# Optimization experiments

Measured on AMD Instinct MI355X. Metric: run time of the kernel, lower is better.

Reference implementation:

```python
import jax, jax.numpy as jnp
import numpy as np

D = 1024
H = 16
DH = D // H  # 64
EPS_LN = 1e-5
CONF_MIN = 1e-6


def sparsemax(z):
    """Sparsemax along the last axis (Martins & Astudillo 2016)."""
    K = z.shape[-1]
    z_sorted = jnp.flip(jnp.sort(z, axis=-1), axis=-1)          # descending
    cssv = jnp.cumsum(z_sorted, axis=-1)                        # cumulative sums
    r = jnp.arange(1, K + 1, dtype=z.dtype)                     # 1..K
    support = (1.0 + r * z_sorted) > cssv                       # bool mask
    k = jnp.sum(support, axis=-1, keepdims=True)                # support size
    tau = (jnp.take_along_axis(cssv, k.astype(jnp.int32) - 1, axis=-1) - 1.0) / k.astype(z.dtype)
    return jnp.maximum(z - tau, 0.0)


def setup_inputs() -> dict:
    key = jax.random.key(0)
    ks = jax.random.split(key, 16)
    B, P, K = 8, 512, 16
    s = 0.02
    return {
        "cell_query": jax.random.normal(ks[0], (B, D), jnp.float32),
        "gene_facets": jax.random.normal(ks[1], (B, P, K, D), jnp.float32),
        "confidence": jax.random.uniform(ks[2], (B, P, K), jnp.float32),
        "wq": jax.random.normal(ks[3], (D, D), jnp.float32) * s,
        "bq": jnp.zeros((D,), jnp.float32),
        "wk": jax.random.normal(ks[4], (D, D), jnp.float32) * s,
        "bk": jnp.zeros((D,), jnp.float32),
        "wv": jax.random.normal(ks[5], (D, D), jnp.float32) * s,
        "bv": jnp.zeros((D,), jnp.float32),
        "wo": jax.random.normal(ks[6], (D, D), jnp.float32) * s,
        "bo": jnp.zeros((D,), jnp.float32),
        "gamma": jnp.ones((D,), jnp.float32),
        "beta": jnp.zeros((D,), jnp.float32),
    }


def reference(cell_query, gene_facets, confidence,
              wq, bq, wk, bk, wv, bv, wo, bo, gamma, beta):
    B = gene_facets.shape[0]
    P = gene_facets.shape[1]
    Kf = gene_facets.shape[2]

    # Projections (torch Linear: x @ W^T + b; here weights stored already transposed as (D,D))
    Q = (cell_query @ wq + bq).reshape(B, H, DH)                       # (B,H,d)
    Kp = (gene_facets @ wk + bk).reshape(B, P, Kf, H, DH)              # (B,P,K,H,d)
    Vp = (gene_facets @ wv + bv).reshape(B, P, Kf, H, DH)              # (B,P,K,H,d)

    # scores: (B,P,H,K)
    scores = jnp.einsum('bhd,bpkhd->bphk', Q, Kp) / jnp.sqrt(jnp.asarray(DH, Q.dtype))
    conf_bias = jnp.log(jnp.clip(confidence, CONF_MIN))                # (B,P,K)
    scores = scores + conf_bias[:, :, None, :]

    alpha = sparsemax(scores)                                          # (B,P,H,K), dropout_p=0 -> identity

    out = jnp.einsum('bphk,bpkhd->bphd', alpha, Vp).reshape(B, P, D)
    out = out @ wo + bo

    # LayerNorm over last dim
    mu = jnp.mean(out, axis=-1, keepdims=True)
    var = jnp.mean((out - mu) ** 2, axis=-1, keepdims=True)
    out = (out - mu) * jax.lax.rsqrt(var + EPS_LN) * gamma + beta
    return out, alpha
```

## Files before the change

kernel.cpp:

```cpp
#include <hip/hip_runtime.h>


typedef float f32x4 __attribute__((ext_vector_type(4)));
typedef short s16x4 __attribute__((ext_vector_type(4)));
typedef short s16x8 __attribute__((ext_vector_type(8)));

__device__ __forceinline__ unsigned short f2bf(float f) {
  unsigned u = __builtin_bit_cast(unsigned, f);
  u = (u + 0x7FFFu + ((u >> 16) & 1u)) >> 16;
  return (unsigned short)u;
}

__device__ __forceinline__ s16x8 pack8(s16x4 lo, s16x4 hi) {
  s16x8 r;
  r[0] = lo[0]; r[1] = lo[1]; r[2] = lo[2]; r[3] = lo[3];
  r[4] = hi[0]; r[5] = hi[1]; r[6] = hi[2]; r[7] = hi[3];
  return r;
}

__global__ __launch_bounds__(256) void k_trans(
    const float* __restrict__ wv, const float* __restrict__ wo,
    unsigned short* __restrict__ wvt, unsigned short* __restrict__ wot) {
  __shared__ float ts[64][65];
  int bid = blockIdx.x;
  const float* src = (bid < 256) ? wv : wo;
  unsigned short* dst = (bid < 256) ? wvt : wot;
  int tile = bid & 255;
  int er = (tile >> 4) << 6;
  int cb = (tile & 15) << 6;
  int t = threadIdx.x;
  int r = t >> 2, c0 = (t & 3) << 4;
#pragma unroll
  for (int j = 0; j < 16; j += 4) {
    f32x4 v = *(const f32x4*)&src[(long)(er + r) * 1024 + cb + c0 + j];
    ts[r][c0 + j + 0] = v[0];
    ts[r][c0 + j + 1] = v[1];
    ts[r][c0 + j + 2] = v[2];
    ts[r][c0 + j + 3] = v[3];
  }
  __syncthreads();
  s16x8 o0, o1;
#pragma unroll
  for (int j = 0; j < 8; ++j) o0[j] = (short)f2bf(ts[c0 + j][r]);
#pragma unroll
  for (int j = 0; j < 8; ++j) o1[j] = (short)f2bf(ts[c0 + 8 + j][r]);
  long ob = (long)(cb + r) * 1024 + er + c0;
  *(s16x8*)&dst[ob] = o0;
  *(s16x8*)&dst[ob + 8] = o1;
}

__global__ __launch_bounds__(256) void k_qpart(
    const float* __restrict__ cq, const float* __restrict__ wq,
    float* __restrict__ qpart) {
  int eq = blockIdx.x, t = threadIdx.x;
  int d0 = t << 2;
  f32x4 acc[8] = {};
  for (int i = 0; i < 64; ++i) {
    int e = (eq << 6) + i;
    f32x4 w = *(const f32x4*)&wq[(long)e * 1024 + d0];
#pragma unroll
    for (int b = 0; b < 8; ++b) acc[b] += w * cq[(b << 10) + e];
  }
#pragma unroll
  for (int b = 0; b < 8; ++b)
    *(f32x4*)&qpart[(long)((b << 4) + eq) * 1024 + d0] = acc[b];
}

__global__ __launch_bounds__(256) void k_wtilde(
    const float* __restrict__ wk, const float* __restrict__ bk,
    const float* __restrict__ bq, const float* __restrict__ qpart,
    unsigned short* __restrict__ wt, float* __restrict__ cvec) {
  __shared__ float Qs[16][68];
  int et = blockIdx.x, b = blockIdx.y, t = threadIdx.x;
#pragma unroll
  for (int j = 0; j < 4; ++j) {
    int d = t + (j << 8);
    float s = bq[d];
    for (int q = 0; q < 16; ++q) s += qpart[(long)((b << 4) + q) * 1024 + d];
    Qs[d >> 6][d & 63] = s;
  }
  __syncthreads();
  int h = t & 15, el = t >> 4;
#pragma unroll
  for (int ii = 0; ii < 8; ++ii) {
    int e = (et << 7) + (ii << 4) + el;
    const float* wr = &wk[(long)e * 1024 + (h << 6)];
    float s = 0.f;
#pragma unroll
    for (int d = 0; d < 64; d += 4) {
      f32x4 w = *(const f32x4*)&wr[d];
      s += w[0] * Qs[h][d] + w[1] * Qs[h][d + 1] + w[2] * Qs[h][d + 2] + w[3] * Qs[h][d + 3];
    }
    wt[(long)((b << 4) + h) * 1024 + e] = f2bf(s);
  }
  if (et == 0 && t < 16) {
    float s = 0.f;
    for (int d = 0; d < 64; ++d) s += bk[(t << 6) + d] * Qs[t][d];
    cvec[(b << 4) + t] = s;
  }
}

#define GSTR 1028
#define TSTR 20
__global__ __launch_bounds__(256, 2) void k_scores(
    const float* __restrict__ G, const float* __restrict__ conf,
    const unsigned short* __restrict__ wt, const float* __restrict__ cvec,
    float* __restrict__ alpha_out, unsigned short* __restrict__ gbar,
    int b0, int hstride) {
  __shared__ short Gs[16 * GSTR];
  __shared__ short Gt[1024 * TSTR];
  __shared__ short As[16 * 32];
  __shared__ float ps[1024];
  __shared__ float lc[16];

  int t = threadIdx.x;
  int lane = t & 63, w = t >> 6;
  int l15 = lane & 15, g4 = lane >> 4;
  int bp = blockIdx.x;
  long gbp = (long)b0 * 512 + bp;
  int b = (int)(gbp >> 9);
  const float* Grow = G + gbp * 16384;
  const unsigned short* wtb = wt + (long)b * 16384;

#pragma unroll
  for (int half = 0; half < 2; ++half) {
    s16x4 col[8];
#pragma unroll
    for (int j = 0; j < 8; ++j) {
      int k = (half << 3) + j;
      f32x4 g = *(const f32x4*)&Grow[(k << 10) + (t << 2)];
      s16x4 h4;
      h4[0] = (short)f2bf(g[0]); h4[1] = (short)f2bf(g[1]);
      h4[2] = (short)f2bf(g[2]); h4[3] = (short)f2bf(g[3]);
      *(s16x4*)&Gs[k * GSTR + (t << 2)] = h4;
      col[j] = h4;
    }
#pragma unroll
    for (int q = 0; q < 4; ++q) {
      int e = (t << 2) + q;
      s16x4 lo, hi;
      lo[0] = col[0][q]; lo[1] = col[1][q]; lo[2] = col[2][q]; lo[3] = col[3][q];
      hi[0] = col[4][q]; hi[1] = col[5][q]; hi[2] = col[6][q]; hi[3] = col[7][q];
      *(s16x4*)&Gt[e * TSTR + (half << 3)] = lo;
      *(s16x4*)&Gt[e * TSTR + (half << 3) + 4] = hi;
    }
  }
  if (t < 16) lc[t] = logf(fmaxf(conf[gbp * 16 + t], 1e-6f));
  __syncthreads();

  f32x4 sc = {0.f, 0.f, 0.f, 0.f};
#pragma unroll
  for (int i = 0; i < 8; ++i) {
    int e0 = (w << 8) + (i << 5) + (g4 << 3);
    s16x8 af = *(const s16x8*)&wtb[l15 * 1024 + e0];
    int off = l15 * GSTR + e0;
    s16x8 bf = pack8(*(const s16x4*)&Gs[off], *(const s16x4*)&Gs[off + 4]);
    sc = __builtin_amdgcn_mfma_f32_16x16x32_bf16(af, bf, sc, 0, 0, 0);
  }
#pragma unroll
  for (int r = 0; r < 4; ++r)
    ps[(w << 8) + ((g4 << 2) + r) * 16 + l15] = sc[r];
  __syncthreads();

  {
    int h = t >> 4, k = t & 15;
    float z = (ps[h * 16 + k] + ps[256 + h * 16 + k] + ps[512 + h * 16 + k] +
               ps[768 + h * 16 + k] + cvec[b * 16 + h]) * 0.125f + lc[k];
    float v = z;
#pragma unroll
    for (int kk = 2; kk <= 16; kk <<= 1) {
#pragma unroll
      for (int j = kk >> 1; j > 0; j >>= 1) {
        float o = __shfl_xor(v, j, 64);
        bool dirDesc = ((l15 & kk) == 0);
        bool takeMax = (((l15 & j) == 0) == dirDesc);
        v = takeMax ? fmaxf(v, o) : fminf(v, o);
      }
    }
    float cs = v;
#pragma unroll
    for (int d = 1; d < 16; d <<= 1) {
      float o = __shfl_up(cs, (unsigned)d, 16);
      if (l15 >= d) cs += o;
    }
    bool sup = (1.0f + (float)(l15 + 1) * v) > cs;
    unsigned long long m = __ballot(sup);
    int gb16 = lane & 48;
    int ksup = (int)__popcll((m >> gb16) & 0xFFFFull);
    float csk = __shfl(cs, ksup - 1, 16);
    float tau = (csk - 1.0f) / (float)ksup;
    float a = fmaxf(z - tau, 0.0f);
    alpha_out[((gbp << 4) + h) * 16 + k] = a;
    As[(h << 5) + k] = (short)f2bf(a);
    As[(h << 5) + 16 + k] = 0;
  }
  __syncthreads();

  s16x8 ab = *(const s16x8*)&As[(l15 << 5) + (g4 << 3)];
#pragma unroll 4
  for (int i = 0; i < 16; ++i) {
    int ebase = ((w << 4) + i) << 4;
    int ro = (ebase + l15) * TSTR + ((g4 & 1) << 3);
    s16x8 aa = pack8(*(const s16x4*)&Gt[ro], *(const s16x4*)&Gt[ro + 4]);
    f32x4 d2 = __builtin_amdgcn_mfma_f32_16x16x32_bf16(
        aa, ab, (f32x4){0.f, 0.f, 0.f, 0.f}, 0, 0, 0);
    s16x4 o4;
    o4[0] = (short)f2bf(d2[0]); o4[1] = (short)f2bf(d2[1]);
    o4[2] = (short)f2bf(d2[2]); o4[3] = (short)f2bf(d2[3]);
    *(s16x4*)&gbar[(long)l15 * hstride + (long)bp * 1024 + ebase + (g4 << 2)] = o4;
  }
}

__global__ __launch_bounds__(256) void k_av(
    const unsigned short* __restrict__ gbar, const unsigned short* __restrict__ wvt,
    const float* __restrict__ bv, unsigned short* __restrict__ av,
    int b0, int hstride) {
  __shared__ short Asm[128 * 40];
  __shared__ short Bsm[64 * 40];
  int t = threadIdx.x;
  int lane = t & 63, w = t >> 6;
  int l15 = lane & 15, g4 = lane >> 4;
  int wm = w >> 1, wn = w & 1;
  int tile = blockIdx.x, h = blockIdx.y;
  const unsigned short* Ab = gbar + (long)h * hstride + (long)tile * 128 * 1024;
  const unsigned short* Bb = wvt + (long)(h << 6) * 1024;
  int ar = t >> 1, ac = (t & 1) << 4;
  int br = t >> 2, bc = (t & 3) << 3;
  const unsigned short* Arp = Ab + (long)ar * 1024 + ac;
  const unsigned short* Brp = Bb + (long)br * 1024 + bc;
  s16x8 a0 = *(const s16x8*)&Arp[0];
  s16x8 a1 = *(const s16x8*)&Arp[8];
  s16x8 b8 = *(const s16x8*)&Brp[0];
  f32x4 acc[4][2] = {};
  for (int kb = 0; kb < 32; ++kb) {
    __syncthreads();
    short* pa = &Asm[ar * 40 + ac];
    *(s16x8*)pa = a0; *(s16x8*)(pa + 8) = a1;
    *(s16x8*)&Bsm[br * 40 + bc] = b8;
    if (kb + 1 < 32) {
      a0 = *(const s16x8*)&Arp[((kb + 1) << 5)];
      a1 = *(const s16x8*)&Arp[((kb + 1) << 5) + 8];
      b8 = *(const s16x8*)&Brp[((kb + 1) << 5)];
    }
    __syncthreads();
    s16x8 afr[4], bfr[2];
#pragma unroll
    for (int im = 0; im < 4; ++im)
      afr[im] = *(const s16x8*)&Asm[(wm * 64 + im * 16 + l15) * 40 + (g4 << 3)];
#pragma unroll
    for (int in = 0; in < 2; ++in)
      bfr[in] = *(const s16x8*)&Bsm[(wn * 32 + in * 16 + l15) * 40 + (g4 << 3)];
#pragma unroll
    for (int im = 0; im < 4; ++im)
#pragma unroll
      for (int in = 0; in < 2; ++in)
        acc[im][in] = __builtin_amdgcn_mfma_f32_16x16x32_bf16(afr[im], bfr[in], acc[im][in], 0, 0, 0);
  }
  long grow0 = (long)b0 * 512 + (long)tile * 128 + wm * 64 + (g4 << 2);
#pragma unroll
  for (int in = 0; in < 2; ++in) {
    int colg = (h << 6) + wn * 32 + in * 16 + l15;
    float bvv = bv[colg];
#pragma unroll
    for (int im = 0; im < 4; ++im) {
      long rowg = grow0 + im * 16;
#pragma unroll
      for (int r = 0; r < 4; ++r)
        av[(rowg + r) * 1024 + colg] = f2bf(acc[im][in][r] + bvv);
    }
  }
}

__global__ __launch_bounds__(256) void k_out(
    const unsigned short* __restrict__ av, const unsigned short* __restrict__ wot,
    const float* __restrict__ bo, float* __restrict__ y) {
  __shared__ short Asm[128 * 40];
  __shared__ short Bsm[128 * 40];
  int mt = blockIdx.x, nt = blockIdx.y, t = threadIdx.x;
  int lane = t & 63, w = t >> 6;
  int wm = w >> 1, wn = w & 1;
  int l15 = lane & 15, g4 = lane >> 4;
  f32x4 acc[4][4] = {};
  int lr = t >> 1, ls = (t & 1) << 4;
  const unsigned short* Ar = av + ((long)(mt * 128 + lr)) * 1024;
  const unsigned short* Br = wot + ((long)(nt * 128 + lr)) * 1024;
  s16x8 a0 = *(const s16x8*)&Ar[ls];
  s16x8 a1 = *(const s16x8*)&Ar[ls + 8];
  s16x8 b0 = *(const s16x8*)&Br[ls];
  s16x8 b1 = *(const s16x8*)&Br[ls + 8];
  for (int kb = 0; kb < 32; ++kb) {
    __syncthreads();
    short* pa = &Asm[lr * 40 + ls];
    *(s16x8*)pa = a0; *(s16x8*)(pa + 8) = a1;
    short* pb = &Bsm[lr * 40 + ls];
    *(s16x8*)pb = b0; *(s16x8*)(pb + 8) = b1;
    if (kb + 1 < 32) {
      a0 = *(const s16x8*)&Ar[((kb + 1) << 5) + ls];
      a1 = *(const s16x8*)&Ar[((kb + 1) << 5) + ls + 8];
      b0 = *(const s16x8*)&Br[((kb + 1) << 5) + ls];
      b1 = *(const s16x8*)&Br[((kb + 1) << 5) + ls + 8];
    }
    __syncthreads();
    s16x8 afr[4], bfr[4];
#pragma unroll
    for (int im = 0; im < 4; ++im)
      afr[im] = *(const s16x8*)&Asm[(wm * 64 + im * 16 + l15) * 40 + (g4 << 3)];
#pragma unroll
    for (int in = 0; in < 4; ++in)
      bfr[in] = *(const s16x8*)&Bsm[(wn * 64 + in * 16 + l15) * 40 + (g4 << 3)];
#pragma unroll
    for (int im = 0; im < 4; ++im)
#pragma unroll
      for (int in = 0; in < 4; ++in)
        acc[im][in] = __builtin_amdgcn_mfma_f32_16x16x32_bf16(afr[im], bfr[in], acc[im][in], 0, 0, 0);
  }
#pragma unroll
  for (int in = 0; in < 4; ++in) {
    int colg = nt * 128 + wn * 64 + in * 16 + l15;
    float bov = bo[colg];
#pragma unroll
    for (int im = 0; im < 4; ++im) {
      long rowg = mt * 128 + wm * 64 + im * 16 + (g4 << 2);
#pragma unroll
      for (int r = 0; r < 4; ++r)
        y[(rowg + r) * 1024 + colg] = acc[im][in][r] + bov;
    }
  }
}

__global__ __launch_bounds__(256) void k_ln(
    float* __restrict__ y, const float* __restrict__ gamma,
    const float* __restrict__ beta) {
  int row = (blockIdx.x << 2) + (threadIdx.x >> 6);
  int lane = threadIdx.x & 63;
  float* yr = y + ((long)row << 10);
  f32x4 v[4];
  float s = 0.f, s2 = 0.f;
#pragma unroll
  for (int j = 0; j < 4; ++j) {
    v[j] = *(const f32x4*)&yr[(lane << 2) + (j << 8)];
#pragma unroll
    for (int q = 0; q < 4; ++q) { s += v[j][q]; s2 += v[j][q] * v[j][q]; }
  }
#pragma unroll
  for (int d = 1; d < 64; d <<= 1) {
    s += __shfl_xor(s, d, 64);
    s2 += __shfl_xor(s2, d, 64);
  }
  float mu = s * (1.0f / 1024.0f);
  float var = s2 * (1.0f / 1024.0f) - mu * mu;
  float rs = rsqrtf(var + 1e-5f);
#pragma unroll
  for (int j = 0; j < 4; ++j) {
    int f0 = (lane << 2) + (j << 8);
    f32x4 gm = *(const f32x4*)&gamma[f0];
    f32x4 bt = *(const f32x4*)&beta[f0];
    f32x4 o;
#pragma unroll
    for (int q = 0; q < 4; ++q) o[q] = (v[j][q] - mu) * rs * gm[q] + bt[q];
    *(f32x4*)&yr[f0] = o;
  }
}

extern "C" void kernel_launch(void* const* d_in, const int* in_sizes, int n_in,
                              void* d_out, int out_size, void* d_ws, size_t ws_size,
                              hipStream_t stream) {
  (void)in_sizes; (void)n_in; (void)out_size;
  const float* cq    = (const float*)d_in[0];
  const float* G     = (const float*)d_in[1];
  const float* conf  = (const float*)d_in[2];
  const float* wq    = (const float*)d_in[3];
  const float* bq    = (const float*)d_in[4];
  const float* wk    = (const float*)d_in[5];
  const float* bk    = (const float*)d_in[6];
  const float* wv    = (const float*)d_in[7];
  const float* bv    = (const float*)d_in[8];
  const float* wo    = (const float*)d_in[9];
  const float* bo    = (const float*)d_in[10];
  const float* gamma = (const float*)d_in[11];
  const float* beta  = (const float*)d_in[12];

  float* y = (float*)d_out;
  float* alpha = y + 4194304;

  char* p = (char*)d_ws;
  float* qpart = (float*)p;                  p += 8L * 16 * 1024 * 4;
  float* cvec  = (float*)p;                  p += 1024;
  unsigned short* wt   = (unsigned short*)p; p += 8L * 16 * 1024 * 2;
  unsigned short* wvt  = (unsigned short*)p; p += 1024L * 1024 * 2;
  unsigned short* wot  = (unsigned short*)p; p += 1024L * 1024 * 2;
  unsigned short* av   = (unsigned short*)p; p += 4096L * 1024 * 2;
  unsigned short* gbar = (unsigned short*)p;
  size_t used = (size_t)(p - (char*)d_ws);
  size_t per_b = 512L * 16 * 1024 * 2;
  int nb = 1;
  if (ws_size >= used + 8 * per_b) nb = 8;
  else if (ws_size >= used + 4 * per_b) nb = 4;
  else if (ws_size >= used + 2 * per_b) nb = 2;
  int hstride = nb * 512 * 1024;

  hipLaunchKernelGGL(k_trans, dim3(512), dim3(256), 0, stream, wv, wo, wvt, wot);
  hipLaunchKernelGGL(k_qpart, dim3(16), dim3(256), 0, stream, cq, wq, qpart);
  hipLaunchKernelGGL(k_wtilde, dim3(8, 8), dim3(256), 0, stream, wk, bk, bq, qpart, wt, cvec);
  for (int c = 0; c < 8; c += nb) {
    hipLaunchKernelGGL(k_scores, dim3(nb * 512), dim3(256), 0, stream,
                       G, conf, wt, cvec, alpha, gbar, c, hstride);
    hipLaunchKernelGGL(k_av, dim3(nb * 4, 16), dim3(256), 0, stream,
                       gbar, wvt, bv, av, c, hstride);
  }
  hipLaunchKernelGGL(k_out, dim3(32, 8), dim3(256), 0, stream, av, wot, bo, y);
  hipLaunchKernelGGL(k_ln, dim3(1024), dim3(256), 0, stream, y, gamma, beta);
}
```

Baseline: 232.6 us.

## Fuse transpose with q-projection, drop transposed G copy, fuse output GEMM with LayerNorm

Three changes. The weight transpose and q-partial kernels are merged into one launch. k_scores no longer builds a transposed bf16 copy of G in shared memory; it reads columns of Gs with strided scalar loads, which cuts LDS use and raises the occupancy hint to 4 blocks. The output GEMM and LayerNorm become a single kernel: each block owns 16 full rows, keeps all 1024 outputs in registers, and reduces the row statistics in-block. This removes the y round trip, but the new GEMM reads wot directly from global memory with no shared-memory tiling, and the scalar LDS gathers may cause bank conflicts.

```diff
diff --git a/kernel.cpp b/kernel.cpp
--- a/kernel.cpp
+++ b/kernel.cpp
@@ -18,52 +18,52 @@
   return r;
 }
 
-__global__ __launch_bounds__(256) void k_trans(
+__global__ __launch_bounds__(256) void k_transq(
     const float* __restrict__ wv, const float* __restrict__ wo,
-    unsigned short* __restrict__ wvt, unsigned short* __restrict__ wot) {
-  __shared__ float ts[64][65];
-  int bid = blockIdx.x;
-  const float* src = (bid < 256) ? wv : wo;
-  unsigned short* dst = (bid < 256) ? wvt : wot;
-  int tile = bid & 255;
-  int er = (tile >> 4) << 6;
-  int cb = (tile & 15) << 6;
-  int t = threadIdx.x;
-  int r = t >> 2, c0 = (t & 3) << 4;
-#pragma unroll
-  for (int j = 0; j < 16; j += 4) {
-    f32x4 v = *(const f32x4*)&src[(long)(er + r) * 1024 + cb + c0 + j];
-    ts[r][c0 + j + 0] = v[0];
-    ts[r][c0 + j + 1] = v[1];
-    ts[r][c0 + j + 2] = v[2];
-    ts[r][c0 + j + 3] = v[3];
-  }
-  __syncthreads();
-  s16x8 o0, o1;
-#pragma unroll
-  for (int j = 0; j < 8; ++j) o0[j] = (short)f2bf(ts[c0 + j][r]);
-#pragma unroll
-  for (int j = 0; j < 8; ++j) o1[j] = (short)f2bf(ts[c0 + 8 + j][r]);
-  long ob = (long)(cb + r) * 1024 + er + c0;
-  *(s16x8*)&dst[ob] = o0;
-  *(s16x8*)&dst[ob + 8] = o1;
-}
-
-__global__ __launch_bounds__(256) void k_qpart(
+    unsigned short* __restrict__ wvt, unsigned short* __restrict__ wot,
     const float* __restrict__ cq, const float* __restrict__ wq,
     float* __restrict__ qpart) {
-  int eq = blockIdx.x, t = threadIdx.x;
-  int d0 = t << 2;
-  f32x4 acc[8] = {};
-  for (int i = 0; i < 64; ++i) {
-    int e = (eq << 6) + i;
-    f32x4 w = *(const f32x4*)&wq[(long)e * 1024 + d0];
-#pragma unroll
-    for (int b = 0; b < 8; ++b) acc[b] += w * cq[(b << 10) + e];
-  }
-#pragma unroll
-  for (int b = 0; b < 8; ++b)
-    *(f32x4*)&qpart[(long)((b << 4) + eq) * 1024 + d0] = acc[b];
+  int bid = blockIdx.x;
+  int t = threadIdx.x;
+  if (bid < 512) {
+    __shared__ float ts[64][65];
+    const float* src = (bid < 256) ? wv : wo;
+    unsigned short* dst = (bid < 256) ? wvt : wot;
+    int tile = bid & 255;
+    int er = (tile >> 4) << 6;
+    int cb = (tile & 15) << 6;
+    int r = t >> 2, c0 = (t & 3) << 4;
+#pragma unroll
+    for (int j = 0; j < 16; j += 4) {
+      f32x4 v = *(const f32x4*)&src[(long)(er + r) * 1024 + cb + c0 + j];
+      ts[r][c0 + j + 0] = v[0];
+      ts[r][c0 + j + 1] = v[1];
+      ts[r][c0 + j + 2] = v[2];
+      ts[r][c0 + j + 3] = v[3];
+    }
+    __syncthreads();
+    s16x8 o0, o1;
+#pragma unroll
+    for (int j = 0; j < 8; ++j) o0[j] = (short)f2bf(ts[c0 + j][r]);
+#pragma unroll
+    for (int j = 0; j < 8; ++j) o1[j] = (short)f2bf(ts[c0 + 8 + j][r]);
+    long ob = (long)(cb + r) * 1024 + er + c0;
+    *(s16x8*)&dst[ob] = o0;
+    *(s16x8*)&dst[ob + 8] = o1;
+  } else {
+    int eq = bid - 512;
+    int d0 = t << 2;
+    f32x4 acc[8] = {};
+    for (int i = 0; i < 64; ++i) {
+      int e = (eq << 6) + i;
+      f32x4 w = *(const f32x4*)&wq[(long)e * 1024 + d0];
+#pragma unroll
+      for (int b = 0; b < 8; ++b) acc[b] += w * cq[(b << 10) + e];
+    }
+#pragma unroll
+    for (int b = 0; b < 8; ++b)
+      *(f32x4*)&qpart[(long)((b << 4) + eq) * 1024 + d0] = acc[b];
+  }
 }
 
 __global__ __launch_bounds__(256) void k_wtilde(
@@ -101,14 +101,12 @@
 }
 
 #define GSTR 1028
-#define TSTR 20
-__global__ __launch_bounds__(256, 2) void k_scores(
+__global__ __launch_bounds__(256, 4) void k_scores(
     const float* __restrict__ G, const float* __restrict__ conf,
     const unsigned short* __restrict__ wt, const float* __restrict__ cvec,
     float* __restrict__ alpha_out, unsigned short* __restrict__ gbar,
     int b0, int hstride) {
   __shared__ short Gs[16 * GSTR];
-  __shared__ short Gt[1024 * TSTR];
   __shared__ short As[16 * 32];
   __shared__ float ps[1024];
   __shared__ float lc[16];
@@ -122,28 +120,13 @@
   const float* Grow = G + gbp * 16384;
   const unsigned short* wtb = wt + (long)b * 16384;
 
-#pragma unroll
-  for (int half = 0; half < 2; ++half) {
-    s16x4 col[8];
-#pragma unroll
-    for (int j = 0; j < 8; ++j) {
-      int k = (half << 3) + j;
-      f32x4 g = *(const f32x4*)&Grow[(k << 10) + (t << 2)];
-      s16x4 h4;
-      h4[0] = (short)f2bf(g[0]); h4[1] = (short)f2bf(g[1]);
-      h4[2] = (short)f2bf(g[2]); h4[3] = (short)f2bf(g[3]);
-      *(s16x4*)&Gs[k * GSTR + (t << 2)] = h4;
-      col[j] = h4;
-    }
-#pragma unroll
-    for (int q = 0; q < 4; ++q) {
-      int e = (t << 2) + q;
-      s16x4 lo, hi;
-      lo[0] = col[0][q]; lo[1] = col[1][q]; lo[2] = col[2][q]; lo[3] = col[3][q];
-      hi[0] = col[4][q]; hi[1] = col[5][q]; hi[2] = col[6][q]; hi[3] = col[7][q];
-      *(s16x4*)&Gt[e * TSTR + (half << 3)] = lo;
-      *(s16x4*)&Gt[e * TSTR + (half << 3) + 4] = hi;
-    }
+#pragma unroll 4
+  for (int k = 0; k < 16; ++k) {
+    f32x4 g = *(const f32x4*)&Grow[(k << 10) + (t << 2)];
+    s16x4 h4;
+    h4[0] = (short)f2bf(g[0]); h4[1] = (short)f2bf(g[1]);
+    h4[2] = (short)f2bf(g[2]); h4[3] = (short)f2bf(g[3]);
+    *(s16x4*)&Gs[k * GSTR + (t << 2)] = h4;
   }
   if (t < 16) lc[t] = logf(fmaxf(conf[gbp * 16 + t], 1e-6f));
   __syncthreads();
@@ -197,11 +180,14 @@
   __syncthreads();
 
   s16x8 ab = *(const s16x8*)&As[(l15 << 5) + (g4 << 3)];
+  int kf0 = (g4 & 1) << 3;
 #pragma unroll 4
   for (int i = 0; i < 16; ++i) {
     int ebase = ((w << 4) + i) << 4;
-    int ro = (ebase + l15) * TSTR + ((g4 & 1) << 3);
-    s16x8 aa = pack8(*(const s16x4*)&Gt[ro], *(const s16x4*)&Gt[ro + 4]);
+    int eA = ebase + l15;
+    s16x8 aa;
+#pragma unroll
+    for (int j = 0; j < 8; ++j) aa[j] = Gs[(kf0 + j) * GSTR + eA];
     f32x4 d2 = __builtin_amdgcn_mfma_f32_16x16x32_bf16(
         aa, ab, (f32x4){0.f, 0.f, 0.f, 0.f}, 0, 0, 0);
     s16x4 o4;
@@ -271,94 +257,86 @@
   }
 }
 
-__global__ __launch_bounds__(256) void k_out(
+__global__ __launch_bounds__(256) void k_outln(
     const unsigned short* __restrict__ av, const unsigned short* __restrict__ wot,
-    const float* __restrict__ bo, float* __restrict__ y) {
-  __shared__ short Asm[128 * 40];
-  __shared__ short Bsm[128 * 40];
-  int mt = blockIdx.x, nt = blockIdx.y, t = threadIdx.x;
+    const float* __restrict__ bo, const float* __restrict__ gamma,
+    const float* __restrict__ beta, float* __restrict__ y) {
+  __shared__ short Asm[16 * 1032];
+  __shared__ float red_s[16][4];
+  __shared__ float red_s2[16][4];
+  int mt = blockIdx.x, t = threadIdx.x;
   int lane = t & 63, w = t >> 6;
-  int wm = w >> 1, wn = w & 1;
   int l15 = lane & 15, g4 = lane >> 4;
-  f32x4 acc[4][4] = {};
-  int lr = t >> 1, ls = (t & 1) << 4;
-  const unsigned short* Ar = av + ((long)(mt * 128 + lr)) * 1024;
-  const unsigned short* Br = wot + ((long)(nt * 128 + lr)) * 1024;
-  s16x8 a0 = *(const s16x8*)&Ar[ls];
-  s16x8 a1 = *(const s16x8*)&Ar[ls + 8];
-  s16x8 b0 = *(const s16x8*)&Br[ls];
-  s16x8 b1 = *(const s16x8*)&Br[ls + 8];
+  const unsigned short* Ab = av + (long)mt * 16 * 1024;
+
+#pragma unroll
+  for (int c = 0; c < 8; ++c) {
+    int flat = (c << 11) + (t << 3);
+    int r = flat >> 10, col = flat & 1023;
+    s16x8 v = *(const s16x8*)&Ab[flat];
+    *(s16x8*)&Asm[r * 1032 + col] = v;
+  }
+  __syncthreads();
+
+  f32x4 acc[16] = {};
   for (int kb = 0; kb < 32; ++kb) {
-    __syncthreads();
-    short* pa = &Asm[lr * 40 + ls];
-    *(s16x8*)pa = a0; *(s16x8*)(pa + 8) = a1;
-    short* pb = &Bsm[lr * 40 + ls];
-    *(s16x8*)pb = b0; *(s16x8*)(pb + 8) = b1;
-    if (kb + 1 < 32) {
-      a0 = *(const s16x8*)&Ar[((kb + 1) << 5) + ls];
-      a1 = *(const s16x8*)&Ar[((kb + 1) << 5) + ls + 8];
-      b0 = *(const s16x8*)&Br[((kb + 1) << 5) + ls];
-      b1 = *(const s16x8*)&Br[((kb + 1) << 5) + ls + 8];
-    }
-    __syncthreads();
-    s16x8 afr[4], bfr[4];
-#pragma unroll
-    for (int im = 0; im < 4; ++im)
-      afr[im] = *(const s16x8*)&Asm[(wm * 64 + im * 16 + l15) * 40 + (g4 << 3)];
-#pragma unroll
-    for (int in = 0; in < 4; ++in)
-      bfr[in] = *(const s16x8*)&Bsm[(wn * 64 + in * 16 + l15) * 40 + (g4 << 3)];
-#pragma unroll
-    for (int im = 0; im < 4; ++im)
-#pragma unroll
-      for (int in = 0; in < 4; ++in)
-        acc[im][in] = __builtin_amdgcn_mfma_f32_16x16x32_bf16(afr[im], bfr[in], acc[im][in], 0, 0, 0);
-  }
-#pragma unroll
-  for (int in = 0; in < 4; ++in) {
-    int colg = nt * 128 + wn * 64 + in * 16 + l15;
-    float bov = bo[colg];
-#pragma unroll
-    for (int im = 0; im < 4; ++im) {
-      long rowg = mt * 128 + wm * 64 + im * 16 + (g4 << 2);
-#pragma unroll
-      for (int r = 0; r < 4; ++r)
-        y[(rowg + r) * 1024 + colg] = acc[im][in][r] + bov;
-    }
-  }
-}
-
-__global__ __launch_bounds__(256) void k_ln(
-    float* __restrict__ y, const float* __restrict__ gamma,
-    const float* __restrict__ beta) {
-  int row = (blockIdx.x << 2) + (threadIdx.x >> 6);
-  int lane = threadIdx.x & 63;
-  float* yr = y + ((long)row << 10);
-  f32x4 v[4];
-  float s = 0.f, s2 = 0.f;
-#pragma unroll
-  for (int j = 0; j < 4; ++j) {
-    v[j] = *(const f32x4*)&yr[(lane << 2) + (j << 8)];
-#pragma unroll
-    for (int q = 0; q < 4; ++q) { s += v[j][q]; s2 += v[j][q] * v[j][q]; }
-  }
-#pragma unroll
-  for (int d = 1; d < 64; d <<= 1) {
-    s += __shfl_xor(s, d, 64);
-    s2 += __shfl_xor(s2, d, 64);
-  }
-  float mu = s * (1.0f / 1024.0f);
-  float var = s2 * (1.0f / 1024.0f) - mu * mu;
-  float rs = rsqrtf(var + 1e-5f);
-#pragma unroll
-  for (int j = 0; j < 4; ++j) {
-    int f0 = (lane << 2) + (j << 8);
-    f32x4 gm = *(const f32x4*)&gamma[f0];
-    f32x4 bt = *(const f32x4*)&beta[f0];
-    f32x4 o;
-#pragma unroll
-    for (int q = 0; q < 4; ++q) o[q] = (v[j][q] - mu) * rs * gm[q] + bt[q];
-    *(f32x4*)&yr[f0] = o;
+    s16x8 af = *(const s16x8*)&Asm[l15 * 1032 + (kb << 5) + (g4 << 3)];
+    s16x8 bf[16];
+#pragma unroll
+    for (int nt = 0; nt < 16; ++nt) {
+      int n = (w << 8) + (nt << 4) + l15;
+      bf[nt] = *(const s16x8*)&wot[(long)n * 1024 + (kb << 5) + (g4 << 3)];
+    }
+#pragma unroll
+    for (int nt = 0; nt < 16; ++nt)
+      acc[nt] = __builtin_amdgcn_mfma_f32_16x16x32_bf16(af, bf[nt], acc[nt], 0, 0, 0);
+  }
+
+  float bov[16];
+#pragma unroll
+  for (int nt = 0; nt < 16; ++nt) bov[nt] = bo[(w << 8) + (nt << 4) + l15];
+  float s[4] = {0.f, 0.f, 0.f, 0.f}, s2[4] = {0.f, 0.f, 0.f, 0.f};
+#pragma unroll
+  for (int nt = 0; nt < 16; ++nt)
+#pragma unroll
+    for (int r = 0; r < 4; ++r) {
+      float o = acc[nt][r] + bov[nt];
+      s[r] += o; s2[r] += o * o;
+    }
+#pragma unroll
+  for (int r = 0; r < 4; ++r)
+#pragma unroll
+    for (int d = 1; d < 16; d <<= 1) {
+      s[r] += __shfl_xor(s[r], d, 16);
+      s2[r] += __shfl_xor(s2[r], d, 16);
+    }
+  if (l15 == 0) {
+#pragma unroll
+    for (int r = 0; r < 4; ++r) {
+      red_s[(g4 << 2) + r][w] = s[r];
+      red_s2[(g4 << 2) + r][w] = s2[r];
+    }
+  }
+  __syncthreads();
+  float mu[4], rs[4];
+#pragma unroll
+  for (int r = 0; r < 4; ++r) {
+    int row = (g4 << 2) + r;
+    float S = red_s[row][0] + red_s[row][1] + red_s[row][2] + red_s[row][3];
+    float S2 = red_s2[row][0] + red_s2[row][1] + red_s2[row][2] + red_s2[row][3];
+    mu[r] = S * (1.0f / 1024.0f);
+    float var = S2 * (1.0f / 1024.0f) - mu[r] * mu[r];
+    rs[r] = rsqrtf(var + 1e-5f);
+  }
+#pragma unroll
+  for (int nt = 0; nt < 16; ++nt) {
+    int c = (w << 8) + (nt << 4) + l15;
+    float gm = gamma[c], bt = beta[c];
+#pragma unroll
+    for (int r = 0; r < 4; ++r) {
+      float o = acc[nt][r] + bov[nt];
+      y[(long)(mt * 16 + (g4 << 2) + r) * 1024 + c] = (o - mu[r]) * rs[r] * gm + bt;
+    }
   }
 }
 
@@ -399,8 +377,8 @@
   else if (ws_size >= used + 2 * per_b) nb = 2;
   int hstride = nb * 512 * 1024;
 
-  hipLaunchKernelGGL(k_trans, dim3(512), dim3(256), 0, stream, wv, wo, wvt, wot);
-  hipLaunchKernelGGL(k_qpart, dim3(16), dim3(256), 0, stream, cq, wq, qpart);
+  hipLaunchKernelGGL(k_transq, dim3(528), dim3(256), 0, stream,
+                     wv, wo, wvt, wot, cq, wq, qpart);
   hipLaunchKernelGGL(k_wtilde, dim3(8, 8), dim3(256), 0, stream, wk, bk, bq, qpart, wt, cvec);
   for (int c = 0; c < 8; c += nb) {
     hipLaunchKernelGGL(k_scores, dim3(nb * 512), dim3(256), 0, stream,
@@ -408,6 +386,6 @@
     hipLaunchKernelGGL(k_av, dim3(nb * 4, 16), dim3(256), 0, stream,
                        gbar, wvt, bv, av, c, hstride);
   }
-  hipLaunchKernelGGL(k_out, dim3(32, 8), dim3(256), 0, stream, av, wot, bo, y);
-  hipLaunchKernelGGL(k_ln, dim3(1024), dim3(256), 0, stream, y, gamma, beta);
-}
+  hipLaunchKernelGGL(k_outln, dim3(256), dim3(256), 0, stream,
+                     av, wot, bo, gamma, beta, y);
+}
```

Result: slower. 299.4 us (+28.7%).
